# Kernel tuning notes

Measured on AMD Instinct MI355X. Metric: run time of the kernel, lower is better.

The kernel has to match this reference:

```python
import jax, jax.numpy as jnp
import numpy as np

D_MODEL = 1024
NHEAD = 16
HEAD_DIM = D_MODEL // NHEAD
EPS = 1e-8


def setup_inputs() -> dict:
    key = jax.random.key(0)
    ks = jax.random.split(key, 10)
    B, T = 2, 2048
    s = 1.0 / np.sqrt(D_MODEL)
    return {
        "query": jax.random.normal(ks[0], (B, T, D_MODEL), jnp.float32),
        "key": jax.random.normal(ks[1], (B, T, D_MODEL), jnp.float32),
        "value": jax.random.normal(ks[2], (B, T, D_MODEL), jnp.float32),
        "frac": jax.random.uniform(ks[3], (B, T), jnp.float32),
        "Wq": jax.random.normal(ks[4], (D_MODEL, D_MODEL), jnp.float32) * s,
        "bq": jnp.zeros((D_MODEL,), jnp.float32),
        "Wk": jax.random.normal(ks[5], (D_MODEL, D_MODEL), jnp.float32) * s,
        "bk": jnp.zeros((D_MODEL,), jnp.float32),
        "Wv": jax.random.normal(ks[6], (D_MODEL, D_MODEL), jnp.float32) * s,
        "bv": jnp.zeros((D_MODEL,), jnp.float32),
        "attn_bias": jax.random.normal(ks[7], (HEAD_DIM,), jnp.float32) * 0.02,
        "Wo": jax.random.normal(ks[8], (D_MODEL, D_MODEL), jnp.float32) * s,
        "bo": jnpp if False else jnp.zeros((D_MODEL,), jnp.float32),
    }


def reference(query, key, value, frac, Wq, bq, Wk, bk, Wv, bv, attn_bias, Wo, bo):
    B, T, _ = query.shape
    H, Dh = NHEAD, HEAD_DIM
    scale = Dh ** -0.5

    # torch Linear: x @ W.T + b
    Q = (query @ Wq.T + bq).reshape(B, T, H, Dh).transpose(0, 2, 1, 3)  # [B,H,T,Dh]
    K = (key @ Wk.T + bk).reshape(B, T, H, Dh).transpose(0, 2, 1, 3)
    V = (value @ Wv.T + bv).reshape(B, T, H, Dh).transpose(0, 2, 1, 3)

    # factor_ij = (frac_j - frac_i) / (frac_i*frac_j + eps), shape [B,T,T]
    fi = frac[:, :, None]
    fj = frac[:, None, :]
    factor = (fj - fi) / (fi * fj + EPS)

    # sum_d (Q_i*K_j + attn_bias*factor)_d == QK^T + sum(attn_bias)*factor
    bias_sum = jnp.sum(attn_bias)
    logits = jnp.einsum('bhid,bhjd->bhij', Q, K) + bias_sum * factor[:, None, :, :]
    logits = logits * scale

    probs = jax.nn.softmax(logits, axis=-1)  # dropout p=0.0 (eval)
    out = jnp.einsum('bhij,bhjd->bhid', probs, V)  # [B,H,T,Dh]
    out = out.transpose(0, 2, 1, 3).reshape(B, T, H * Dh)
    return out @ Wo.T + bo
```

## Files before the change

### kernel.cpp

```cpp
#include <hip/hip_runtime.h>

typedef short s16x8 __attribute__((ext_vector_type(8)));
typedef float f32x4 __attribute__((ext_vector_type(4)));
typedef unsigned int u32x2 __attribute__((ext_vector_type(2)));
typedef unsigned short u16;
typedef unsigned int u32;

#define D_MODEL 1024
#define NHEAD   16
#define HD      64
#define TSEQ    2048
#define NB      2
#define MROWS   4096

#define LOG2E 1.4426950408889634f
#define QSCALE (0.125f * LOG2E)

__device__ __forceinline__ u16 f2bf(float f) {
  unsigned u = __builtin_bit_cast(unsigned, f);
  u += 0x7fffu + ((u >> 16) & 1u);
  return (u16)(u >> 16);
}

__device__ __forceinline__ u32 cvtpk(float lo, float hi) {
  u32 r;
  asm("v_cvt_pk_bf16_f32 %0, %1, %2" : "=v"(r) : "v"(lo), "v"(hi));
  return r;
}

__device__ __forceinline__ float exp2fast(float x) {
#if __has_builtin(__builtin_amdgcn_exp2f)
  return __builtin_amdgcn_exp2f(x);
#else
  return exp2f(x);
#endif
}

__device__ __forceinline__ float rcpfast(float x) {
#if __has_builtin(__builtin_amdgcn_rcpf)
  return __builtin_amdgcn_rcpf(x);
#else
  return 1.f / x;
#endif
}

__device__ __forceinline__ void gload16(const void* g, void* l) {
  __builtin_amdgcn_global_load_lds((const __attribute__((address_space(1))) void*)g,
                                   (__attribute__((address_space(3))) void*)l,
                                   16, 0, 0);
}

__global__ void cvt3(const float* __restrict__ a, const float* __restrict__ b,
                     const float* __restrict__ c, u16* o0, u16* o1, u16* o2, int n4) {
  int i = blockIdx.x * blockDim.x + threadIdx.x;
  if (i >= n4) return;
  const float* in = (blockIdx.y == 0) ? a : (blockIdx.y == 1) ? b : c;
  u16* out = (blockIdx.y == 0) ? o0 : (blockIdx.y == 1) ? o1 : o2;
  float4 v = ((const float4*)in)[i];
  ushort4 o;
  o.x = f2bf(v.x); o.y = f2bf(v.y); o.z = f2bf(v.z); o.w = f2bf(v.w);
  ((ushort4*)out)[i] = o;
}

__global__ void cvt4(const float* __restrict__ a, const float* __restrict__ b,
                     const float* __restrict__ c, const float* __restrict__ d,
                     u16* o0, u16* o1, u16* o2, u16* o3, int n4) {
  int i = blockIdx.x * blockDim.x + threadIdx.x;
  if (i >= n4) return;
  int z = blockIdx.y;
  const float* in = (z == 0) ? a : (z == 1) ? b : (z == 2) ? c : d;
  u16* out = (z == 0) ? o0 : (z == 1) ? o1 : (z == 2) ? o2 : o3;
  float4 v = ((const float4*)in)[i];
  ushort4 o;
  o.x = f2bf(v.x); o.y = f2bf(v.y); o.z = f2bf(v.z); o.w = f2bf(v.w);
  ((ushort4*)out)[i] = o;
}

__global__ void bias_sum_k(const float* __restrict__ ab, float* __restrict__ o) {
  float v = ab[threadIdx.x];
#pragma unroll
  for (int m = 32; m >= 1; m >>= 1) v += __shfl_xor(v, m);
  if (threadIdx.x == 0) o[0] = v;
}

#define GEMM_BODY(A_, Bt_, bias_, out_, mode_, oscale_)                                  \
  constexpr int K = 1024, N = 1024;                                                      \
  int tid = threadIdx.x;                                                                 \
  int wid = tid >> 6, lane = tid & 63;                                                   \
  int l15 = lane & 15, lgp = lane >> 4;                                                  \
  int wr = wid >> 1, wc = wid & 1;                                                       \
  int m0 = blockIdx.y * 128, n0 = blockIdx.x * 128;                                      \
  int r0 = tid & 127, c0 = tid >> 7;                                                     \
  const u16* gA0 = A_ + (size_t)(m0 + r0) * K + c0 * 8;                                  \
  const u16* gA1 = A_ + (size_t)(m0 + r0) * K + (c0 + 2) * 8;                            \
  const u16* gB0 = Bt_ + (size_t)(n0 + r0) * K + c0 * 8;                                 \
  const u16* gB1 = Bt_ + (size_t)(n0 + r0) * K + (c0 + 2) * 8;                           \
  u16* lA0 = &lA[0][0][0] + (size_t)(wid * 64) * 8;                                      \
  u16* lA1 = &lA[0][0][0] + (size_t)(256 + wid * 64) * 8;                                \
  u16* lB0 = &lB[0][0][0] + (size_t)(wid * 64) * 8;                                      \
  u16* lB1 = &lB[0][0][0] + (size_t)(256 + wid * 64) * 8;                                \
  f32x4 acc[4][4];                                                                       \
  _Pragma("unroll") for (int m = 0; m < 4; ++m)                                          \
    _Pragma("unroll") for (int n = 0; n < 4; ++n)                                        \
      acc[m][n] = (f32x4){0.f, 0.f, 0.f, 0.f};                                           \
  for (int k0 = 0; k0 < K; k0 += 32) {                                                   \
    gload16(gA0 + k0, lA0);                                                              \
    gload16(gA1 + k0, lA1);                                                              \
    gload16(gB0 + k0, lB0);                                                              \
    gload16(gB1 + k0, lB1);                                                              \
    __syncthreads();                                                                     \
    s16x8 af[4], bf[4];                                                                  \
    _Pragma("unroll") for (int m = 0; m < 4; ++m)                                        \
      af[m] = *(const s16x8*)&lA[lgp][wr * 64 + m * 16 + l15][0];                        \
    _Pragma("unroll") for (int n = 0; n < 4; ++n)                                        \
      bf[n] = *(const s16x8*)&lB[lgp][wc * 64 + n * 16 + l15][0];                        \
    _Pragma("unroll") for (int m = 0; m < 4; ++m)                                        \
      _Pragma("unroll") for (int n = 0; n < 4; ++n)                                      \
        acc[m][n] = __builtin_amdgcn_mfma_f32_16x16x32_bf16(af[m], bf[n], acc[m][n], 0, 0, 0); \
    __syncthreads();                                                                     \
  }                                                                                      \
  float bvv[4];                                                                          \
  _Pragma("unroll") for (int n = 0; n < 4; ++n)                                          \
    bvv[n] = bias_[n0 + wc * 64 + n * 16 + l15];                                         \
  _Pragma("unroll") for (int m = 0; m < 4; ++m) {                                        \
    int rowb = m0 + wr * 64 + m * 16 + lgp * 4;                                          \
    _Pragma("unroll") for (int n = 0; n < 4; ++n) {                                      \
      int col = n0 + wc * 64 + n * 16 + l15;                                             \
      _Pragma("unroll") for (int r = 0; r < 4; ++r) {                                    \
        int row = rowb + r;                                                              \
        float v = (acc[m][n][r] + bvv[n]) * oscale_;                                     \
        if (mode_ == 2) {                                                                \
          ((float*)out_)[(size_t)row * N + col] = v;                                     \
        } else {                                                                         \
          int b = row >> 11, t = row & 2047;                                             \
          int h = col >> 6, d = col & 63;                                                \
          u16 x = f2bf(v);                                                               \
          if (mode_ == 0)                                                                \
            ((u16*)out_)[(((size_t)(b * NHEAD + h) * TSEQ + t) << 6) + d] = x;           \
          else                                                                           \
            ((u16*)out_)[(((size_t)(b * NHEAD + h) * HD + d) << 11) + t] = x;            \
        }                                                                                \
      }                                                                                  \
    }                                                                                    \
  }

__global__ __launch_bounds__(256) void gemm_qkv(const u16* __restrict__ qb, const u16* __restrict__ kb,
                                                const u16* __restrict__ vb,
                                                const u16* __restrict__ Wqb, const u16* __restrict__ Wkb,
                                                const u16* __restrict__ Wvb,
                                                const float* __restrict__ bq, const float* __restrict__ bk,
                                                const float* __restrict__ bv,
                                                u16* Qp, u16* Kp, u16* Vtp) {
  __shared__ __align__(16) u16 lA[4][128][8];
  __shared__ __align__(16) u16 lB[4][128][8];
  int z = blockIdx.z;
  const u16* A = (z == 0) ? qb : (z == 1) ? kb : vb;
  const u16* Bt = (z == 0) ? Wqb : (z == 1) ? Wkb : Wvb;
  const float* bias = (z == 0) ? bq : (z == 1) ? bk : bv;
  u16* out = (z == 0) ? Qp : (z == 1) ? Kp : Vtp;
  int mode = (z == 2) ? 1 : 0;
  float oscale = (z == 0) ? QSCALE : 1.0f;
  GEMM_BODY(A, Bt, bias, out, mode, oscale)
}

__global__ __launch_bounds__(256) void gemm_out(const u16* __restrict__ A, const u16* __restrict__ Bt,
                                                const float* __restrict__ bias, float* __restrict__ out) {
  __shared__ __align__(16) u16 lA[4][128][8];
  __shared__ __align__(16) u16 lB[4][128][8];
  GEMM_BODY(A, Bt, bias, out, 2, 1.0f)
}

__global__ __launch_bounds__(256, 4) void attn_kernel(const u16* __restrict__ Qp,
                                                      const u16* __restrict__ Kp,
                                                      const u16* __restrict__ Vt,
                                                      const float* __restrict__ frac,
                                                      const float* __restrict__ bsum,
                                                      u16* __restrict__ aout) {
  __shared__ __align__(16) u16 kbuf[2][64 * 64];
  __shared__ __align__(16) u16 vbuf[2][64 * 64];
  __shared__ __align__(16) u16 plds[4][16 * 64];
  const int tid = threadIdx.x, wid = tid >> 6, lane = tid & 63;
  const int l15 = lane & 15, lgp = lane >> 4;
  const int bh = blockIdx.y, b = bh >> 4, h = bh & 15;
  const u16* Qh = Qp + (size_t)bh * TSEQ * HD;
  const u16* Kh = Kp + (size_t)bh * TSEQ * HD;
  const u16* Vh = Vt + (size_t)bh * HD * TSEQ;
  const float* fb = frac + b * TSEQ;
  const float bs = bsum[0] * 0.125f * LOG2E;
  const float THR2 = 24.0f;
  const int q0 = blockIdx.x * 64 + wid * 16;

  const int srow = lane >> 3;
  const int sg8 = ((lane & 7) ^ srow) * 8;
  const int rbase = wid * 8 + srow;

  const int ofs0 = l15 * 64 + ((lgp ^ (l15 & 7)) * 8);
  const int ofs1 = l15 * 64 + (((4 + lgp) ^ (l15 & 7)) * 8);

  s16x8 qf[2];
#pragma unroll
  for (int ks = 0; ks < 2; ++ks)
    qf[ks] = *(const s16x8*)(Qh + (size_t)(q0 + l15) * HD + ks * 32 + lgp * 8);

  const float fi = fb[q0 + l15];
  const float nbfi = -bs * fi;
  float m2run = -1e30f;
  float lsum = 0.f;
  f32x4 o[4];
#pragma unroll
  for (int nd = 0; nd < 4; ++nd) o[nd] = (f32x4){0.f, 0.f, 0.f, 0.f};

  auto stage = [&](int buf, int t) {
    int kv0s = t * 64;
#pragma unroll
    for (int i = 0; i < 2; ++i) {
      int row = i * 32 + rbase;
      gload16(Kh + (size_t)(kv0s + row) * HD + sg8, &kbuf[buf][i * 2048 + wid * 512]);
      gload16(Vh + (size_t)row * TSEQ + kv0s + sg8, &vbuf[buf][i * 2048 + wid * 512]);
    }
  };

  int cur = 0;
  stage(0, 0);
  float4 fj_cur[4], fj_nxt[4];
#pragma unroll
  for (int n = 0; n < 4; ++n) fj_cur[n] = *(const float4*)(fb + n * 16 + lgp * 4);
  __syncthreads();

  for (int t = 0; t < TSEQ / 64; ++t) {
    const bool more = (t + 1 < TSEQ / 64);
    if (more) {
      stage(cur ^ 1, t + 1);
#pragma unroll
      for (int n = 0; n < 4; ++n)
        fj_nxt[n] = *(const float4*)(fb + (t + 1) * 64 + n * 16 + lgp * 4);
    }

    const u16* kb = &kbuf[cur][0];
    const u16* vb = &vbuf[cur][0];

    f32x4 s[4];
#pragma unroll
    for (int n = 0; n < 4; ++n) {
      s16x8 kf0 = *(const s16x8*)(kb + n * 1024 + ofs0);
      s16x8 kf1 = *(const s16x8*)(kb + n * 1024 + ofs1);
      f32x4 a = (f32x4){0.f, 0.f, 0.f, 0.f};
      a = __builtin_amdgcn_mfma_f32_16x16x32_bf16(kf0, qf[0], a, 0, 0, 0);
      a = __builtin_amdgcn_mfma_f32_16x16x32_bf16(kf1, qf[1], a, 0, 0, 0);
      s[n] = a;
    }

    float pmax = -1e30f;
#pragma unroll
    for (int n = 0; n < 4; ++n) {
#pragma unroll
      for (int r = 0; r < 4; ++r) {
        float fj = (r == 0) ? fj_cur[n].x : (r == 1) ? fj_cur[n].y : (r == 2) ? fj_cur[n].z : fj_cur[n].w;
        float num = __builtin_fmaf(bs, fj, nbfi);
        float den = __builtin_fmaf(fi, fj, 1e-8f);
        float l2 = __builtin_fmaf(num, rcpfast(den), s[n][r]);
        s[n][r] = l2;
        pmax = fmaxf(pmax, l2);
      }
    }

    if (__any((pmax - m2run) > THR2)) {
      float tm = fmaxf(pmax, __shfl_xor(pmax, 16));
      tm = fmaxf(tm, __shfl_xor(tm, 32));
      float m2n = fmaxf(m2run, tm);
      float alpha = exp2fast(m2run - m2n);
      lsum *= alpha;
      m2run = m2n;
      float af[4];
#pragma unroll
      for (int r = 0; r < 4; ++r) af[r] = __shfl(alpha, lgp * 4 + r);
#pragma unroll
      for (int nd = 0; nd < 4; ++nd)
#pragma unroll
        for (int r = 0; r < 4; ++r) o[nd][r] *= af[r];
    }

    u32 w[4][2];
    {
      float ps = 0.f;
#pragma unroll
      for (int n = 0; n < 4; ++n) {
#pragma unroll
        for (int s2 = 0; s2 < 2; ++s2) {
          float p0 = exp2fast(s[n][2 * s2 + 0] - m2run);
          float p1 = exp2fast(s[n][2 * s2 + 1] - m2run);
          ps += p0 + p1;
          w[n][s2] = cvtpk(p0, p1);
        }
      }
      lsum += ps;
    }

    u16* pw = &plds[wid][0];
#pragma unroll
    for (int n = 0; n < 4; ++n) {
      int idx = l15 * 64 + ((n * 16 + lgp * 4) ^ ((l15 & 7) << 3));
      *(u32x2*)(pw + idx) = (u32x2){w[n][0], w[n][1]};
    }
    s16x8 pf[2];
#pragma unroll
    for (int ks = 0; ks < 2; ++ks) {
      int idx = l15 * 64 + ((ks * 32 + lgp * 8) ^ ((l15 & 7) << 3));
      pf[ks] = *(const s16x8*)(pw + idx);
    }

#pragma unroll
    for (int nd = 0; nd < 4; ++nd) {
      s16x8 vf0 = *(const s16x8*)(vb + nd * 1024 + ofs0);
      s16x8 vf1 = *(const s16x8*)(vb + nd * 1024 + ofs1);
      o[nd] = __builtin_amdgcn_mfma_f32_16x16x32_bf16(pf[0], vf0, o[nd], 0, 0, 0);
      o[nd] = __builtin_amdgcn_mfma_f32_16x16x32_bf16(pf[1], vf1, o[nd], 0, 0, 0);
    }

    __syncthreads();
    cur ^= 1;
    if (more) {
#pragma unroll
      for (int n = 0; n < 4; ++n) fj_cur[n] = fj_nxt[n];
    }
  }

  {
    float l = lsum;
    l += __shfl_xor(l, 16);
    l += __shfl_xor(l, 32);
    float rl[4];
#pragma unroll
    for (int r = 0; r < 4; ++r) rl[r] = __fdividef(1.f, __shfl(l, lgp * 4 + r));
#pragma unroll
    for (int nd = 0; nd < 4; ++nd)
#pragma unroll
      for (int r = 0; r < 4; ++r) {
        int q = q0 + lgp * 4 + r;
        aout[((size_t)(b * TSEQ + q)) * D_MODEL + h * HD + nd * 16 + l15] = f2bf(o[nd][r] * rl[r]);
      }
  }
}

extern "C" void kernel_launch(void* const* d_in, const int* in_sizes, int n_in,
                              void* d_out, int out_size, void* d_ws, size_t ws_size,
                              hipStream_t stream) {
  const float* query = (const float*)d_in[0];
  const float* key_  = (const float*)d_in[1];
  const float* value = (const float*)d_in[2];
  const float* frac  = (const float*)d_in[3];
  const float* Wq    = (const float*)d_in[4];
  const float* bq    = (const float*)d_in[5];
  const float* Wk    = (const float*)d_in[6];
  const float* bk    = (const float*)d_in[7];
  const float* Wv    = (const float*)d_in[8];
  const float* bv    = (const float*)d_in[9];
  const float* abias = (const float*)d_in[10];
  const float* Wo    = (const float*)d_in[11];
  const float* bo    = (const float*)d_in[12];

  char* ws = (char*)d_ws;
  size_t off = 0;
  auto alloc = [&](size_t bytes) { char* p = ws + off; off += (bytes + 255) & ~255ULL; return p; };
  const size_t XB = (size_t)MROWS * D_MODEL * 2;
  const size_t WB = (size_t)D_MODEL * D_MODEL * 2;
  u16* qb  = (u16*)alloc(XB);
  u16* kb  = (u16*)alloc(XB);
  u16* vb  = (u16*)alloc(XB);
  u16* Wqb = (u16*)alloc(WB);
  u16* Wkb = (u16*)alloc(WB);
  u16* Wvb = (u16*)alloc(WB);
  u16* Wob = (u16*)alloc(WB);
  float* bsum = (float*)alloc(256);
  u16* Qp  = (u16*)alloc(XB);
  u16* Kp  = (u16*)alloc(XB);
  u16* Vtp = (u16*)alloc(XB);
  u16* AO  = (u16*)alloc(XB);

  const int n4X = MROWS * D_MODEL / 4;
  const int n4W = D_MODEL * D_MODEL / 4;
  cvt3<<<dim3(n4X / 256, 3), dim3(256), 0, stream>>>(query, key_, value, qb, kb, vb, n4X);
  cvt4<<<dim3(n4W / 256, 4), dim3(256), 0, stream>>>(Wq, Wk, Wv, Wo, Wqb, Wkb, Wvb, Wob, n4W);
  bias_sum_k<<<dim3(1), dim3(64), 0, stream>>>(abias, bsum);

  gemm_qkv<<<dim3(D_MODEL / 128, MROWS / 128, 3), dim3(256), 0, stream>>>(
      qb, kb, vb, Wqb, Wkb, Wvb, bq, bk, bv, Qp, Kp, Vtp);

  attn_kernel<<<dim3(TSEQ / 64, NB * NHEAD), dim3(256), 0, stream>>>(Qp, Kp, Vtp, frac, bsum, AO);

  gemm_out<<<dim3(D_MODEL / 128, MROWS / 128), dim3(256), 0, stream>>>(AO, Wob, bo, (float*)d_out);
}
```

Measured before the change: 192.6 us.

## Fuse conversion kernels, double-buffer GEMM LDS, retile out-proj, add MFMA priority

Merges the three conversion and bias-sum launches into one kernel, with the bias sum prescaled there. Replaces the GEMM macro with a templated core that double-buffers LDS so the next K-slice loads while MFMAs run, removing one barrier per iteration. The output projection moves to 64x128 tiles to launch more blocks. It also wraps the MFMA sections in s_setprio and loads frac values for the current tile inside the attention loop instead of prefetching them. The risks are doubled LDS use in the QKV GEMM, which may reduce occupancy, and frac load latency now sitting on the critical path.

```diff
diff --git a/kernel.cpp b/kernel.cpp
--- a/kernel.cpp
+++ b/kernel.cpp
@@ -50,99 +50,140 @@
                                    16, 0, 0);
 }
 
-__global__ void cvt3(const float* __restrict__ a, const float* __restrict__ b,
-                     const float* __restrict__ c, u16* o0, u16* o1, u16* o2, int n4) {
-  int i = blockIdx.x * blockDim.x + threadIdx.x;
-  if (i >= n4) return;
-  const float* in = (blockIdx.y == 0) ? a : (blockIdx.y == 1) ? b : c;
-  u16* out = (blockIdx.y == 0) ? o0 : (blockIdx.y == 1) ? o1 : o2;
-  float4 v = ((const float4*)in)[i];
+__global__ void cvt_all(const float* __restrict__ q, const float* __restrict__ k,
+                        const float* __restrict__ v, const float* __restrict__ wq,
+                        const float* __restrict__ wk, const float* __restrict__ wv,
+                        const float* __restrict__ wo, const float* __restrict__ ab,
+                        u16* qb, u16* kb, u16* vb, u16* wqb, u16* wkb, u16* wvb, u16* wob,
+                        float* bsum) {
+  if (blockIdx.x == 16384) {
+    if (threadIdx.x < 64) {
+      float s = ab[threadIdx.x];
+#pragma unroll
+      for (int m = 32; m >= 1; m >>= 1) s += __shfl_xor(s, m);
+      if (threadIdx.x == 0) bsum[0] = s * 0.125f * LOG2E;
+    }
+    return;
+  }
+  int i = blockIdx.x * 256 + threadIdx.x;
+  const float* src; u16* dst; int off;
+  if (i < 3 * 1048576) {
+    int t = i >> 20; off = i & 1048575;
+    src = (t == 0) ? q : (t == 1) ? k : v;
+    dst = (t == 0) ? qb : (t == 1) ? kb : vb;
+  } else {
+    int j = i - 3 * 1048576;
+    int t = j >> 18; off = j & 262143;
+    src = (t == 0) ? wq : (t == 1) ? wk : (t == 2) ? wv : wo;
+    dst = (t == 0) ? wqb : (t == 1) ? wkb : (t == 2) ? wvb : wob;
+  }
+  float4 x = ((const float4*)src)[off];
   ushort4 o;
-  o.x = f2bf(v.x); o.y = f2bf(v.y); o.z = f2bf(v.z); o.w = f2bf(v.w);
-  ((ushort4*)out)[i] = o;
-}
-
-__global__ void cvt4(const float* __restrict__ a, const float* __restrict__ b,
-                     const float* __restrict__ c, const float* __restrict__ d,
-                     u16* o0, u16* o1, u16* o2, u16* o3, int n4) {
-  int i = blockIdx.x * blockDim.x + threadIdx.x;
-  if (i >= n4) return;
-  int z = blockIdx.y;
-  const float* in = (z == 0) ? a : (z == 1) ? b : (z == 2) ? c : d;
-  u16* out = (z == 0) ? o0 : (z == 1) ? o1 : (z == 2) ? o2 : o3;
-  float4 v = ((const float4*)in)[i];
-  ushort4 o;
-  o.x = f2bf(v.x); o.y = f2bf(v.y); o.z = f2bf(v.z); o.w = f2bf(v.w);
-  ((ushort4*)out)[i] = o;
-}
-
-__global__ void bias_sum_k(const float* __restrict__ ab, float* __restrict__ o) {
-  float v = ab[threadIdx.x];
-#pragma unroll
-  for (int m = 32; m >= 1; m >>= 1) v += __shfl_xor(v, m);
-  if (threadIdx.x == 0) o[0] = v;
-}
-
-#define GEMM_BODY(A_, Bt_, bias_, out_, mode_, oscale_)                                  \
-  constexpr int K = 1024, N = 1024;                                                      \
-  int tid = threadIdx.x;                                                                 \
-  int wid = tid >> 6, lane = tid & 63;                                                   \
-  int l15 = lane & 15, lgp = lane >> 4;                                                  \
-  int wr = wid >> 1, wc = wid & 1;                                                       \
-  int m0 = blockIdx.y * 128, n0 = blockIdx.x * 128;                                      \
-  int r0 = tid & 127, c0 = tid >> 7;                                                     \
-  const u16* gA0 = A_ + (size_t)(m0 + r0) * K + c0 * 8;                                  \
-  const u16* gA1 = A_ + (size_t)(m0 + r0) * K + (c0 + 2) * 8;                            \
-  const u16* gB0 = Bt_ + (size_t)(n0 + r0) * K + c0 * 8;                                 \
-  const u16* gB1 = Bt_ + (size_t)(n0 + r0) * K + (c0 + 2) * 8;                           \
-  u16* lA0 = &lA[0][0][0] + (size_t)(wid * 64) * 8;                                      \
-  u16* lA1 = &lA[0][0][0] + (size_t)(256 + wid * 64) * 8;                                \
-  u16* lB0 = &lB[0][0][0] + (size_t)(wid * 64) * 8;                                      \
-  u16* lB1 = &lB[0][0][0] + (size_t)(256 + wid * 64) * 8;                                \
-  f32x4 acc[4][4];                                                                       \
-  _Pragma("unroll") for (int m = 0; m < 4; ++m)                                          \
-    _Pragma("unroll") for (int n = 0; n < 4; ++n)                                        \
-      acc[m][n] = (f32x4){0.f, 0.f, 0.f, 0.f};                                           \
-  for (int k0 = 0; k0 < K; k0 += 32) {                                                   \
-    gload16(gA0 + k0, lA0);                                                              \
-    gload16(gA1 + k0, lA1);                                                              \
-    gload16(gB0 + k0, lB0);                                                              \
-    gload16(gB1 + k0, lB1);                                                              \
-    __syncthreads();                                                                     \
-    s16x8 af[4], bf[4];                                                                  \
-    _Pragma("unroll") for (int m = 0; m < 4; ++m)                                        \
-      af[m] = *(const s16x8*)&lA[lgp][wr * 64 + m * 16 + l15][0];                        \
-    _Pragma("unroll") for (int n = 0; n < 4; ++n)                                        \
-      bf[n] = *(const s16x8*)&lB[lgp][wc * 64 + n * 16 + l15][0];                        \
-    _Pragma("unroll") for (int m = 0; m < 4; ++m)                                        \
-      _Pragma("unroll") for (int n = 0; n < 4; ++n)                                      \
-        acc[m][n] = __builtin_amdgcn_mfma_f32_16x16x32_bf16(af[m], bf[n], acc[m][n], 0, 0, 0); \
-    __syncthreads();                                                                     \
-  }                                                                                      \
-  float bvv[4];                                                                          \
-  _Pragma("unroll") for (int n = 0; n < 4; ++n)                                          \
-    bvv[n] = bias_[n0 + wc * 64 + n * 16 + l15];                                         \
-  _Pragma("unroll") for (int m = 0; m < 4; ++m) {                                        \
-    int rowb = m0 + wr * 64 + m * 16 + lgp * 4;                                          \
-    _Pragma("unroll") for (int n = 0; n < 4; ++n) {                                      \
-      int col = n0 + wc * 64 + n * 16 + l15;                                             \
-      _Pragma("unroll") for (int r = 0; r < 4; ++r) {                                    \
-        int row = rowb + r;                                                              \
-        float v = (acc[m][n][r] + bvv[n]) * oscale_;                                     \
-        if (mode_ == 2) {                                                                \
-          ((float*)out_)[(size_t)row * N + col] = v;                                     \
-        } else {                                                                         \
-          int b = row >> 11, t = row & 2047;                                             \
-          int h = col >> 6, d = col & 63;                                                \
-          u16 x = f2bf(v);                                                               \
-          if (mode_ == 0)                                                                \
-            ((u16*)out_)[(((size_t)(b * NHEAD + h) * TSEQ + t) << 6) + d] = x;           \
-          else                                                                           \
-            ((u16*)out_)[(((size_t)(b * NHEAD + h) * HD + d) << 11) + t] = x;            \
-        }                                                                                \
-      }                                                                                  \
-    }                                                                                    \
-  }
+  o.x = f2bf(x.x); o.y = f2bf(x.y); o.z = f2bf(x.z); o.w = f2bf(x.w);
+  ((ushort4*)dst)[off] = o;
+}
+
+template <int BM, int BN, int WN>
+__device__ __forceinline__ void gemm_core(const u16* __restrict__ A, const u16* __restrict__ Bt,
+                                          const float* __restrict__ bias, void* __restrict__ out,
+                                          float oscale, int mode, u16* lds) {
+  constexpr int K = 1024, N = 1024;
+  constexpr int WM = 4 / WN;
+  constexpr int WTM = BM / WM, WTN = BN / WN;
+  constexpr int MR = WTM / 16, NR = WTN / 16;
+  constexpr int ASZ = BM * 32, BSZ = BN * 32;
+  constexpr int AISS = ASZ / 2048, BISS = BSZ / 2048;
+  u16* lA = lds;
+  u16* lB = lds + 2 * ASZ;
+
+  const int tid = threadIdx.x;
+  const int wid = tid >> 6, lane = tid & 63;
+  const int l15 = lane & 15, lgp = lane >> 4;
+  const int wr = wid / WN, wc = wid % WN;
+  const int m0 = blockIdx.y * BM, n0 = blockIdx.x * BN;
+
+  const u16* gA[AISS];
+  const u16* gB[BISS];
+#pragma unroll
+  for (int i = 0; i < AISS; ++i) {
+    int tp = i * 256 + tid, row = tp % BM, kc = tp / BM;
+    gA[i] = A + (size_t)(m0 + row) * K + kc * 8;
+  }
+#pragma unroll
+  for (int i = 0; i < BISS; ++i) {
+    int tp = i * 256 + tid, row = tp % BN, kc = tp / BN;
+    gB[i] = Bt + (size_t)(n0 + row) * K + kc * 8;
+  }
+
+  f32x4 acc[MR][NR];
+#pragma unroll
+  for (int m = 0; m < MR; ++m)
+#pragma unroll
+    for (int n = 0; n < NR; ++n) acc[m][n] = (f32x4){0.f, 0.f, 0.f, 0.f};
+
+  auto stage = [&](int buf, int k0) {
+#pragma unroll
+    for (int i = 0; i < AISS; ++i)
+      gload16(gA[i] + k0, lA + buf * ASZ + (i * 256 + tid) * 8);
+#pragma unroll
+    for (int i = 0; i < BISS; ++i)
+      gload16(gB[i] + k0, lB + buf * BSZ + (i * 256 + tid) * 8);
+  };
+
+  int cur = 0;
+  stage(0, 0);
+  __syncthreads();
+  for (int k0 = 0; k0 < K; k0 += 32) {
+    if (k0 + 32 < K) stage(cur ^ 1, k0 + 32);
+    const u16* a = lA + cur * ASZ;
+    const u16* b = lB + cur * BSZ;
+    s16x8 af[MR], bf[NR];
+#pragma unroll
+    for (int m = 0; m < MR; ++m)
+      af[m] = *(const s16x8*)(a + lgp * BM * 8 + (wr * WTM + m * 16 + l15) * 8);
+#pragma unroll
+    for (int n = 0; n < NR; ++n)
+      bf[n] = *(const s16x8*)(b + lgp * BN * 8 + (wc * WTN + n * 16 + l15) * 8);
+    __builtin_amdgcn_s_setprio(1);
+#pragma unroll
+    for (int m = 0; m < MR; ++m)
+#pragma unroll
+      for (int n = 0; n < NR; ++n)
+        acc[m][n] = __builtin_amdgcn_mfma_f32_16x16x32_bf16(af[m], bf[n], acc[m][n], 0, 0, 0);
+    __builtin_amdgcn_s_setprio(0);
+    __syncthreads();
+    cur ^= 1;
+  }
+
+  float bvv[NR];
+#pragma unroll
+  for (int n = 0; n < NR; ++n) bvv[n] = bias[n0 + wc * WTN + n * 16 + l15];
+
+#pragma unroll
+  for (int m = 0; m < MR; ++m) {
+    int rowb = m0 + wr * WTM + m * 16 + lgp * 4;
+#pragma unroll
+    for (int n = 0; n < NR; ++n) {
+      int col = n0 + wc * WTN + n * 16 + l15;
+#pragma unroll
+      for (int r = 0; r < 4; ++r) {
+        int row = rowb + r;
+        float vv = (acc[m][n][r] + bvv[n]) * oscale;
+        if (mode == 2) {
+          ((float*)out)[(size_t)row * N + col] = vv;
+        } else {
+          int b = row >> 11, t = row & 2047;
+          int h = col >> 6, d = col & 63;
+          u16 x = f2bf(vv);
+          if (mode == 0)
+            ((u16*)out)[(((size_t)(b * NHEAD + h) * TSEQ + t) << 6) + d] = x;
+          else
+            ((u16*)out)[(((size_t)(b * NHEAD + h) * HD + d) << 11) + t] = x;
+        }
+      }
+    }
+  }
+}
 
 __global__ __launch_bounds__(256) void gemm_qkv(const u16* __restrict__ qb, const u16* __restrict__ kb,
                                                 const u16* __restrict__ vb,
@@ -151,23 +192,21 @@
                                                 const float* __restrict__ bq, const float* __restrict__ bk,
                                                 const float* __restrict__ bv,
                                                 u16* Qp, u16* Kp, u16* Vtp) {
-  __shared__ __align__(16) u16 lA[4][128][8];
-  __shared__ __align__(16) u16 lB[4][128][8];
+  __shared__ __align__(16) u16 lds[2 * 128 * 32 * 2];
   int z = blockIdx.z;
-  const u16* A = (z == 0) ? qb : (z == 1) ? kb : vb;
+  const u16* A  = (z == 0) ? qb : (z == 1) ? kb : vb;
   const u16* Bt = (z == 0) ? Wqb : (z == 1) ? Wkb : Wvb;
   const float* bias = (z == 0) ? bq : (z == 1) ? bk : bv;
   u16* out = (z == 0) ? Qp : (z == 1) ? Kp : Vtp;
   int mode = (z == 2) ? 1 : 0;
   float oscale = (z == 0) ? QSCALE : 1.0f;
-  GEMM_BODY(A, Bt, bias, out, mode, oscale)
+  gemm_core<128, 128, 2>(A, Bt, bias, out, oscale, mode, lds);
 }
 
 __global__ __launch_bounds__(256) void gemm_out(const u16* __restrict__ A, const u16* __restrict__ Bt,
                                                 const float* __restrict__ bias, float* __restrict__ out) {
-  __shared__ __align__(16) u16 lA[4][128][8];
-  __shared__ __align__(16) u16 lB[4][128][8];
-  GEMM_BODY(A, Bt, bias, out, 2, 1.0f)
+  __shared__ __align__(16) u16 lds[2 * 64 * 32 + 2 * 128 * 32];
+  gemm_core<64, 128, 4>(A, Bt, bias, out, 1.0f, 2, lds);
 }
 
 __global__ __launch_bounds__(256, 4) void attn_kernel(const u16* __restrict__ Qp,
@@ -186,7 +225,7 @@
   const u16* Kh = Kp + (size_t)bh * TSEQ * HD;
   const u16* Vh = Vt + (size_t)bh * HD * TSEQ;
   const float* fb = frac + b * TSEQ;
-  const float bs = bsum[0] * 0.125f * LOG2E;
+  const float bs = bsum[0];
   const float THR2 = 24.0f;
   const int q0 = blockIdx.x * 64 + wid * 16;
 
@@ -222,24 +261,22 @@
 
   int cur = 0;
   stage(0, 0);
-  float4 fj_cur[4], fj_nxt[4];
-#pragma unroll
-  for (int n = 0; n < 4; ++n) fj_cur[n] = *(const float4*)(fb + n * 16 + lgp * 4);
   __syncthreads();
 
   for (int t = 0; t < TSEQ / 64; ++t) {
     const bool more = (t + 1 < TSEQ / 64);
-    if (more) {
-      stage(cur ^ 1, t + 1);
-#pragma unroll
-      for (int n = 0; n < 4; ++n)
-        fj_nxt[n] = *(const float4*)(fb + (t + 1) * 64 + n * 16 + lgp * 4);
-    }
+    if (more) stage(cur ^ 1, t + 1);
+
+    float4 fj4[4];
+#pragma unroll
+    for (int n = 0; n < 4; ++n)
+      fj4[n] = *(const float4*)(fb + t * 64 + n * 16 + lgp * 4);
 
     const u16* kb = &kbuf[cur][0];
     const u16* vb = &vbuf[cur][0];
 
     f32x4 s[4];
+    __builtin_amdgcn_s_setprio(1);
 #pragma unroll
     for (int n = 0; n < 4; ++n) {
       s16x8 kf0 = *(const s16x8*)(kb + n * 1024 + ofs0);
@@ -249,13 +286,14 @@
       a = __builtin_amdgcn_mfma_f32_16x16x32_bf16(kf1, qf[1], a, 0, 0, 0);
       s[n] = a;
     }
+    __builtin_amdgcn_s_setprio(0);
 
     float pmax = -1e30f;
 #pragma unroll
     for (int n = 0; n < 4; ++n) {
 #pragma unroll
       for (int r = 0; r < 4; ++r) {
-        float fj = (r == 0) ? fj_cur[n].x : (r == 1) ? fj_cur[n].y : (r == 2) ? fj_cur[n].z : fj_cur[n].w;
+        float fj = (r == 0) ? fj4[n].x : (r == 1) ? fj4[n].y : (r == 2) ? fj4[n].z : fj4[n].w;
         float num = __builtin_fmaf(bs, fj, nbfi);
         float den = __builtin_fmaf(fi, fj, 1e-8f);
         float l2 = __builtin_fmaf(num, rcpfast(den), s[n][r]);
@@ -309,6 +347,7 @@
       pf[ks] = *(const s16x8*)(pw + idx);
     }
 
+    __builtin_amdgcn_s_setprio(1);
 #pragma unroll
     for (int nd = 0; nd < 4; ++nd) {
       s16x8 vf0 = *(const s16x8*)(vb + nd * 1024 + ofs0);
@@ -316,13 +355,10 @@
       o[nd] = __builtin_amdgcn_mfma_f32_16x16x32_bf16(pf[0], vf0, o[nd], 0, 0, 0);
       o[nd] = __builtin_amdgcn_mfma_f32_16x16x32_bf16(pf[1], vf1, o[nd], 0, 0, 0);
     }
+    __builtin_amdgcn_s_setprio(0);
 
     __syncthreads();
     cur ^= 1;
-    if (more) {
-#pragma unroll
-      for (int n = 0; n < 4; ++n) fj_cur[n] = fj_nxt[n];
-    }
   }
 
   {
@@ -377,16 +413,13 @@
   u16* Vtp = (u16*)alloc(XB);
   u16* AO  = (u16*)alloc(XB);
 
-  const int n4X = MROWS * D_MODEL / 4;
-  const int n4W = D_MODEL * D_MODEL / 4;
-  cvt3<<<dim3(n4X / 256, 3), dim3(256), 0, stream>>>(query, key_, value, qb, kb, vb, n4X);
-  cvt4<<<dim3(n4W / 256, 4), dim3(256), 0, stream>>>(Wq, Wk, Wv, Wo, Wqb, Wkb, Wvb, Wob, n4W);
-  bias_sum_k<<<dim3(1), dim3(64), 0, stream>>>(abias, bsum);
+  cvt_all<<<dim3(16385), dim3(256), 0, stream>>>(query, key_, value, Wq, Wk, Wv, Wo, abias,
+                                                 qb, kb, vb, Wqb, Wkb, Wvb, Wob, bsum);
 
   gemm_qkv<<<dim3(D_MODEL / 128, MROWS / 128, 3), dim3(256), 0, stream>>>(
       qb, kb, vb, Wqb, Wkb, Wvb, bq, bk, bv, Qp, Kp, Vtp);
 
   attn_kernel<<<dim3(TSEQ / 64, NB * NHEAD), dim3(256), 0, stream>>>(Qp, Kp, Vtp, frac, bsum, AO);
 
-  gemm_out<<<dim3(D_MODEL / 128, MROWS / 128), dim3(256), 0, stream>>>(AO, Wob, bo, (float*)d_out);
-}
+  gemm_out<<<dim3(D_MODEL / 128, MROWS / 64), dim3(256), 0, stream>>>(AO, Wob, bo, (float*)d_out);
+}
```

After: 184.8 us. -4.0%, faster.
